# Kernel optimization log

Measured on AMD Instinct MI355X. Metric: run time of the kernel, lower is better.

## Reference

```python
import jax, jax.numpy as jnp
import numpy as np
import math

B, T, EMB, HD = 4, 2048, 2048, 128
HALF = HD // 2


def setup_inputs() -> dict:
    key = jax.random.key(0)
    ks = jax.random.split(key, 4)
    x = jax.random.normal(ks[0], (B, T, EMB), dtype=jnp.float32)
    s = 1.0 / math.sqrt(EMB)
    Wq = jax.random.normal(ks[1], (EMB, HD), dtype=jnp.float32) * s
    Wk = jax.random.normal(ks[2], (EMB, HD), dtype=jnp.float32) * s
    Wv = jax.random.normal(ks[3], (EMB, HD), dtype=jnp.float32) * s
    # Standard RoPE rotation table: theta_i = 10000^(-2i/HD), angle = pos * theta
    inv_freq = 1.0 / (10000.0 ** (np.arange(0, HALF, dtype=np.float32) / HALF))
    angles = np.arange(T, dtype=np.float32)[:, None] * inv_freq[None, :]  # [T, HALF]
    rot_cos = jnp.asarray(np.cos(angles), dtype=jnp.float32)
    rot_sin = jnp.asarray(np.sin(angles), dtype=jnp.float32)
    # Additive causal mask: 0 on/below diagonal, -1e9 above
    NEG = -1e9
    mask = jnp.where(jnp.tril(jnp.ones((T, T), dtype=bool)), 0.0, NEG).astype(jnp.float32)
    return {"x": x, "Wq": Wq, "Wk": Wk, "Wv": Wv,
            "rot_cos": rot_cos, "rot_sin": rot_sin, "mask": mask}


def _apply_rope(q, rot_cos, rot_sin):
    # q: [B, T, HD]; view last dim as HALF complex pairs and rotate
    qp = q.reshape(q.shape[0], q.shape[1], HALF, 2)
    re, im = qp[..., 0], qp[..., 1]
    out_re = re * rot_cos - im * rot_sin  # broadcast [T,HALF] over batch
    out_im = re * rot_sin + im * rot_cos
    return jnp.stack([out_re, out_im], axis=-1).reshape(q.shape)


def reference(x, Wq, Wk, Wv, rot_cos, rot_sin, mask):
    Q = x @ Wq  # [B, T, HD]
    K = x @ Wk
    V = x @ Wv
    Q = _apply_rope(Q, rot_cos, rot_sin)
    K = _apply_rope(K, rot_cos, rot_sin)
    scores = jnp.einsum('bqd,bkd->bqk', Q, K) / math.sqrt(HD)
    probs = jax.nn.softmax(scores + mask, axis=-1)  # dropout is identity in eval
    return jnp.einsum('bqk,bkd->bqd', probs, V)
```

## Files before the change

kernel.cpp:

```cpp
#include <hip/hip_runtime.h>
#include <cstddef>
#include <cstdint>

#define T_SEQ 2048
#define EMB_D 2048
#define HD_D  128

typedef __attribute__((ext_vector_type(8))) short short8;
typedef __attribute__((ext_vector_type(4))) float f32x4;
typedef __attribute__((ext_vector_type(4))) unsigned short ushort4v;
typedef __attribute__((ext_vector_type(8))) unsigned short ushort8v;
typedef __attribute__((ext_vector_type(2))) unsigned int uint2v;

static __device__ __forceinline__ unsigned short f2bf_rne(float f) {
    union { float f; unsigned u; } v; v.f = f;
    unsigned r = v.u + 0x7fffu + ((v.u >> 16) & 1u);
    return (unsigned short)(r >> 16);
}
static __device__ __forceinline__ unsigned short f2bf_fast(float f) {
    union { float f; unsigned u; } v; v.f = f;
    return (unsigned short)((v.u + 0x8000u) >> 16);
}
static __device__ __forceinline__ float bf2f(unsigned short h) {
    union { unsigned u; float f; } v; v.u = ((unsigned)h) << 16;
    return v.f;
}
static __device__ __forceinline__ unsigned pk2(float a, float b) {
    union { float f; unsigned u; } x, y; x.f = a; y.f = b;
    return __builtin_amdgcn_perm(y.u + 0x8000u, x.u + 0x8000u, 0x07060302);
}
#define EXP2F(x) __builtin_amdgcn_exp2f(x)

__global__ __launch_bounds__(256) void prep_weights(
    const float* __restrict__ Wq, const float* __restrict__ Wk,
    const float* __restrict__ Wv, unsigned short* __restrict__ Wt)
{
    __shared__ __attribute__((aligned(16))) unsigned short tw[64 * 132];
    const int w = blockIdx.y;
    const int k0 = blockIdx.x * 64;
    const float* W = (w == 0) ? Wq : (w == 1) ? Wk : Wv;
    const int tid = threadIdx.x;
#pragma unroll
    for (int p = 0; p < 8; p++) {
        const int f = p * 256 + tid;
        const int row = f >> 5, c4 = f & 31;
        const float4 v = *(const float4*)&W[(size_t)(k0 + row) * HD_D + c4 * 4];
        ushort4v h = { f2bf_rne(v.x), f2bf_rne(v.y), f2bf_rne(v.z), f2bf_rne(v.w) };
        *(ushort4v*)&tw[row * 132 + c4 * 4] = h;
    }
    __syncthreads();
    const int kk = (tid & 7) * 8;
#pragma unroll
    for (int p = 0; p < 4; p++) {
        const int n = p * 32 + (tid >> 3);
        ushort8v o;
#pragma unroll
        for (int jj = 0; jj < 8; jj++) o[jj] = tw[(kk + jj) * 132 + n];
        *(ushort8v*)&Wt[(size_t)w * (HD_D * EMB_D) + (size_t)n * EMB_D + k0 + kk] = o;
    }
}

__global__ __launch_bounds__(256, 2) void qkv_fused(
    const float* __restrict__ x, const unsigned short* __restrict__ Wt,
    const float* __restrict__ rcos, const float* __restrict__ rsin,
    unsigned short* __restrict__ Qb, unsigned short* __restrict__ Kb,
    unsigned short* __restrict__ Vt)
{
    __shared__ __attribute__((aligned(16))) unsigned short xsm[2][64 * 64];
    __shared__ __attribute__((aligned(16))) unsigned short wsm[2][96 * 64];
    const int L = blockIdx.x;
    const int xcd = L & 7, s = L >> 3;
    const int ng = s & 3;
    const int m0 = (xcd * 16 + (s >> 2)) * 64;
    const int tid = threadIdx.x;
    const int lane = tid & 63, wave = tid >> 6;
    const int wm = wave >> 1, wn = wave & 1;
    const int l15 = lane & 15, lq = lane >> 4;

    const int xrow = tid >> 4, xc = tid & 15;
    const float* xsrc = x + (size_t)(m0 + xrow) * EMB_D + xc * 4;
    const int wrow = tid >> 3, wc = tid & 7;
    const unsigned short* wsrc = Wt + (size_t)(ng * 96 + wrow) * EMB_D + wc * 8;

    const int xw  = xrow * 128 + (((xc >> 1) ^ (xrow & 7)) << 4) + (xc & 1) * 8;
    const int wwo = wrow * 128 + ((wc ^ (wrow & 7)) << 4);

    int ra[2][2], rb[3][2];
#pragma unroll
    for (int i = 0; i < 2; i++)
#pragma unroll
        for (int ks = 0; ks < 2; ks++) {
            const int row = wm * 32 + i * 16 + l15;
            ra[i][ks] = row * 128 + (((ks * 4 + lq) ^ (row & 7)) << 4);
        }
#pragma unroll
    for (int jj = 0; jj < 3; jj++)
#pragma unroll
        for (int ks = 0; ks < 2; ks++) {
            const int row = wn * 48 + jj * 16 + l15;
            rb[jj][ks] = row * 128 + (((ks * 4 + lq) ^ (row & 7)) << 4);
        }

    f32x4 acc[2][3];
#pragma unroll
    for (int i = 0; i < 2; i++)
#pragma unroll
        for (int j = 0; j < 3; j++) acc[i][j] = (f32x4){0.f, 0.f, 0.f, 0.f};

    float4 xr[2][4];
    short8 wr[2][3];

#define LOADN(SET, K)                                                             \
    do {                                                                          \
        _Pragma("unroll")                                                         \
        for (int p = 0; p < 4; p++)                                               \
            xr[SET][p] = *(const float4*)(xsrc + (size_t)p * (16 * EMB_D) + (K)); \
        _Pragma("unroll")                                                         \
        for (int p = 0; p < 3; p++)                                               \
            wr[SET][p] = *(const short8*)(wsrc + (size_t)p * (32 * EMB_D) + (K)); \
    } while (0)

#define STAGE(SET, BUF)                                                           \
    do {                                                                          \
        char* xb = (char*)&xsm[BUF][0];                                           \
        char* wb = (char*)&wsm[BUF][0];                                           \
        _Pragma("unroll")                                                         \
        for (int p = 0; p < 4; p++) {                                             \
            uint2v u;                                                             \
            u.x = pk2(xr[SET][p].x, xr[SET][p].y);                                \
            u.y = pk2(xr[SET][p].z, xr[SET][p].w);                                \
            *(uint2v*)(xb + xw + p * 2048) = u;                                   \
        }                                                                         \
        _Pragma("unroll")                                                         \
        for (int p = 0; p < 3; p++)                                               \
            *(short8*)(wb + wwo + p * 4096) = wr[SET][p];                         \
    } while (0)

#define COMPUTE(BUF)                                                              \
    do {                                                                          \
        const char* xb = (const char*)&xsm[BUF][0];                               \
        const char* wb = (const char*)&wsm[BUF][0];                               \
        short8 Af[2][2];                                                          \
        _Pragma("unroll")                                                         \
        for (int i = 0; i < 2; i++)                                               \
            _Pragma("unroll")                                                     \
            for (int ks = 0; ks < 2; ks++)                                        \
                Af[i][ks] = *(const short8*)(xb + ra[i][ks]);                     \
        __builtin_amdgcn_s_setprio(1);                                            \
        _Pragma("unroll")                                                         \
        for (int ks = 0; ks < 2; ks++)                                            \
            _Pragma("unroll")                                                     \
            for (int jj = 0; jj < 3; jj++) {                                      \
                const short8 Bf = *(const short8*)(wb + rb[jj][ks]);              \
                _Pragma("unroll")                                                 \
                for (int i = 0; i < 2; i++)                                       \
                    acc[i][jj] = __builtin_amdgcn_mfma_f32_16x16x32_bf16(         \
                        Af[i][ks], Bf, acc[i][jj], 0, 0, 0);                      \
            }                                                                     \
        __builtin_amdgcn_s_setprio(0);                                            \
    } while (0)

#define BARX() asm volatile("s_waitcnt lgkmcnt(0)\n\ts_barrier" ::: "memory")

    LOADN(0, 0);
    LOADN(1, 64);
    STAGE(0, 0);
    LOADN(0, 128);

#pragma clang loop unroll(disable)
    for (int j = 0; j < 28; j += 2) {
        BARX(); STAGE(1, 1); LOADN(1, (j + 3) * 64); COMPUTE(0);
        BARX(); STAGE(0, 0); LOADN(0, (j + 4) * 64); COMPUTE(1);
    }
    BARX(); STAGE(1, 1); LOADN(1, 31 * 64); COMPUTE(0);
    BARX(); STAGE(0, 0);                    COMPUTE(1);
    BARX(); STAGE(1, 1);                    COMPUTE(0);
    BARX();                                 COMPUTE(1);

#undef LOADN
#undef STAGE
#undef COMPUTE
#undef BARX

    const float qscale = 0.08838834764831845f * 1.4426950408889634f;
#pragma unroll
    for (int i = 0; i < 2; i++) {
#pragma unroll
        for (int r = 0; r < 4; r++) {
            const int row = m0 + wm * 32 + i * 16 + lq * 4 + r;
            const int t = row & (T_SEQ - 1);
            const int bb = row >> 11;
#pragma unroll
            for (int j = 0; j < 3; j++) {
                const int col = ng * 96 + wn * 48 + j * 16 + l15;
                const int mat = col >> 7, mcol = col & 127;
                const float v = acc[i][j][r];
                if (mat == 2) {
                    Vt[((size_t)bb * HD_D + mcol) * T_SEQ + t] = f2bf_rne(v);
                } else {
                    const int ip = mcol >> 1;
                    const float c = rcos[t * 64 + ip];
                    const float s2 = rsin[t * 64 + ip];
                    const float pv = __shfl_xor(v, 1);
                    float rv = (mcol & 1) ? (pv * s2 + v * c) : (v * c - pv * s2);
                    if (mat == 0) {
                        rv *= qscale;
                        Qb[(size_t)row * HD_D + mcol] = f2bf_rne(rv);
                    } else {
                        Kb[(size_t)row * HD_D + mcol] = f2bf_rne(rv);
                    }
                }
            }
        }
    }
}

__global__ __launch_bounds__(256, 2) void attn(
    const unsigned short* __restrict__ Qb, const unsigned short* __restrict__ Kb,
    const unsigned short* __restrict__ Vt, float* __restrict__ O0,
    unsigned short* __restrict__ O1, float* __restrict__ Lp)
{
    __shared__ __attribute__((aligned(16))) unsigned short O_s[4][16 * 128];
    __shared__ __attribute__((aligned(16))) unsigned short P_s[4][2][16 * 40];
    __shared__ float l_s[4][16];

    const int tid = threadIdx.x;
    const int lane = tid & 63, wave = tid >> 6;
    const int l15 = lane & 15, lq = lane >> 4;
    const int kf = lq * 8;

    const int L = blockIdx.x;
    const int g = L & 1;
    const int b = (L >> 1) & 3;
    const int q0 = (127 - (L >> 3)) * 16;
    const int kend = q0 + 16;
    const float M2 = 16.0f;

    const unsigned short* Qp = Qb + (size_t)(b * T_SEQ + q0) * HD_D;
    short8 aQ[4];
#pragma unroll
    for (int d = 0; d < 4; d++)
        aQ[d] = *(const short8*)&Qp[l15 * HD_D + d * 32 + kf];

    f32x4 acc[8];
#pragma unroll
    for (int d = 0; d < 8; d++) acc[d] = (f32x4){0.f, 0.f, 0.f, 0.f};
    float l_r[4] = {0.f, 0.f, 0.f, 0.f};

    const unsigned short* Kbase = Kb + (size_t)b * T_SEQ * HD_D;
    const unsigned short* Vbase = Vt + (size_t)b * HD_D * T_SEQ;
    unsigned short* PwA = &P_s[wave][0][0];
    unsigned short* PwB = &P_s[wave][1][0];

    for (int c = 2 * wave + g; c * 32 < kend; c += 16) {
        const int kA = c * 32;
        const int kB = (c + 8) * 32;
        const bool hB = kB < kend;

        const unsigned short* KpA = Kbase + (size_t)kA * HD_D;
        const unsigned short* KpB = Kbase + (size_t)kB * HD_D;
        short8 KA[8], KB_[8];
#pragma unroll
        for (int d = 0; d < 4; d++)
#pragma unroll
            for (int n = 0; n < 2; n++)
                KA[d * 2 + n] = *(const short8*)&KpA[(size_t)(n * 16 + l15) * HD_D + d * 32 + kf];
        if (hB) {
#pragma unroll
            for (int d = 0; d < 4; d++)
#pragma unroll
                for (int n = 0; n < 2; n++)
                    KB_[d * 2 + n] = *(const short8*)&KpB[(size_t)(n * 16 + l15) * HD_D + d * 32 + kf];
        }

        f32x4 sA0 = (f32x4){0.f, 0.f, 0.f, 0.f}, sA1 = sA0, sB0 = sA0, sB1 = sA0;
#pragma unroll
        for (int d = 0; d < 4; d++) {
            sA0 = __builtin_amdgcn_mfma_f32_16x16x32_bf16(aQ[d], KA[d * 2 + 0], sA0, 0, 0, 0);
            sA1 = __builtin_amdgcn_mfma_f32_16x16x32_bf16(aQ[d], KA[d * 2 + 1], sA1, 0, 0, 0);
        }
        if (hB) {
#pragma unroll
            for (int d = 0; d < 4; d++) {
                sB0 = __builtin_amdgcn_mfma_f32_16x16x32_bf16(aQ[d], KB_[d * 2 + 0], sB0, 0, 0, 0);
                sB1 = __builtin_amdgcn_mfma_f32_16x16x32_bf16(aQ[d], KB_[d * 2 + 1], sB1, 0, 0, 0);
            }
        }

        short8 VA[8];
#pragma unroll
        for (int d = 0; d < 8; d++)
            VA[d] = *(const short8*)&Vbase[(size_t)(d * 16 + l15) * T_SEQ + kA + kf];

#pragma unroll
        for (int r = 0; r < 4; r++) {
            const int q = q0 + lq * 4 + r;
            const float p0 = ((kA + l15)      <= q) ? EXP2F(sA0[r] - M2) : 0.f;
            const float p1 = ((kA + 16 + l15) <= q) ? EXP2F(sA1[r] - M2) : 0.f;
            l_r[r] += p0 + p1;
            const int prow = (lq * 4 + r) * 40;
            PwA[prow + l15]      = f2bf_fast(p0);
            PwA[prow + 16 + l15] = f2bf_fast(p1);
        }
        const short8 pA = *(const short8*)&PwA[l15 * 40 + kf];
#pragma unroll
        for (int d = 0; d < 8; d++)
            acc[d] = __builtin_amdgcn_mfma_f32_16x16x32_bf16(pA, VA[d], acc[d], 0, 0, 0);

        if (hB) {
            short8 VB[8];
#pragma unroll
            for (int d = 0; d < 8; d++)
                VB[d] = *(const short8*)&Vbase[(size_t)(d * 16 + l15) * T_SEQ + kB + kf];
#pragma unroll
            for (int r = 0; r < 4; r++) {
                const int q = q0 + lq * 4 + r;
                const float p0 = ((kB + l15)      <= q) ? EXP2F(sB0[r] - M2) : 0.f;
                const float p1 = ((kB + 16 + l15) <= q) ? EXP2F(sB1[r] - M2) : 0.f;
                l_r[r] += p0 + p1;
                const int prow = (lq * 4 + r) * 40;
                PwB[prow + l15]      = f2bf_fast(p0);
                PwB[prow + 16 + l15] = f2bf_fast(p1);
            }
            const short8 pB = *(const short8*)&PwB[l15 * 40 + kf];
#pragma unroll
            for (int d = 0; d < 8; d++)
                acc[d] = __builtin_amdgcn_mfma_f32_16x16x32_bf16(pB, VB[d], acc[d], 0, 0, 0);
        }
    }

#pragma unroll
    for (int r = 0; r < 4; r++) {
        float lr = l_r[r];
        lr += __shfl_xor(lr, 1);
        lr += __shfl_xor(lr, 2);
        lr += __shfl_xor(lr, 4);
        lr += __shfl_xor(lr, 8);
        if (l15 == 0) l_s[wave][lq * 4 + r] = lr;
#pragma unroll
        for (int d = 0; d < 8; d++)
            O_s[wave][(lq * 4 + r) * 128 + d * 16 + l15] = f2bf_fast(acc[d][r]);
    }
    __syncthreads();

    const int row = tid >> 4;
    const int dc = (tid & 15) * 8;
    const float lt = l_s[0][row] + l_s[1][row] + l_s[2][row] + l_s[3][row];
    float o[8];
#pragma unroll
    for (int k = 0; k < 8; k++) o[k] = 0.f;
#pragma unroll
    for (int w2 = 0; w2 < 4; w2++) {
        const ushort8v pv = *(const ushort8v*)&O_s[w2][row * 128 + dc];
#pragma unroll
        for (int k = 0; k < 8; k++) o[k] += bf2f(pv[k]);
    }
    const size_t grow = (size_t)(b * T_SEQ + q0 + row);
    if (g == 0) {
        float* op = O0 + grow * HD_D + dc;
#pragma unroll
        for (int k = 0; k < 8; k++) op[k] = o[k];
    } else {
        ushort8v h;
#pragma unroll
        for (int k = 0; k < 8; k++) h[k] = f2bf_fast(o[k]);
        *(ushort8v*)&O1[grow * HD_D + dc] = h;
    }
    if ((tid & 15) == 0) Lp[g * 8192 + grow] = lt;
}

__global__ __launch_bounds__(256) void attn_merge(
    float* __restrict__ out, const unsigned short* __restrict__ O1,
    const float* __restrict__ Lp)
{
    const int idx = blockIdx.x * 256 + threadIdx.x;
    const int row = idx >> 5;
    f32x4 a = ((f32x4*)out)[idx];
    const ushort4v h = ((const ushort4v*)O1)[idx];
    f32x4 bv = { bf2f(h.x), bf2f(h.y), bf2f(h.z), bf2f(h.w) };
    const float inv = 1.0f / (Lp[row] + Lp[8192 + row]);
    ((f32x4*)out)[idx] = (a + bv) * inv;
}

extern "C" void kernel_launch(void* const* d_in, const int* in_sizes, int n_in,
                              void* d_out, int out_size, void* d_ws, size_t ws_size,
                              hipStream_t stream)
{
    (void)in_sizes; (void)n_in; (void)out_size; (void)ws_size;
    const float* x  = (const float*)d_in[0];
    const float* Wq = (const float*)d_in[1];
    const float* Wk = (const float*)d_in[2];
    const float* Wv = (const float*)d_in[3];
    const float* rc = (const float*)d_in[4];
    const float* rs = (const float*)d_in[5];
    float* out = (float*)d_out;

    char* ws = (char*)d_ws;
    unsigned short* Wt = (unsigned short*)(ws);
    unsigned short* Qb = (unsigned short*)(ws + 1572864);
    unsigned short* Kb = (unsigned short*)(ws + 3670016);
    unsigned short* Vt = (unsigned short*)(ws + 5767168);
    unsigned short* O1 = (unsigned short*)(ws + 7864320);
    float*          Lp = (float*)(ws + 9961472);

    prep_weights<<<dim3(32, 3), 256, 0, stream>>>(Wq, Wk, Wv, Wt);
    qkv_fused   <<<dim3(512),   256, 0, stream>>>(x, Wt, rc, rs, Qb, Kb, Vt);
    attn        <<<dim3(1024),  256, 0, stream>>>(Qb, Kb, Vt, out, O1, Lp);
    attn_merge  <<<dim3(1024),  256, 0, stream>>>(out, O1, Lp);
}
```

Baseline: 179.9 us.

## Enlarge attention query tile to 32 rows and software-pipeline K loads

Each attention block now handles 32 query rows instead of 16, so every K and V fragment loaded from global memory feeds two MFMA row tiles. The grid is halved to 512 blocks to match. The key loop is restructured with ping-pong K register buffers so the next chunk's K load is issued before the current chunk's softmax and PV step. The cost is more registers (double accumulators and two K buffers) at launch bounds of 2 blocks per CU, fewer blocks for load balancing across the causal triangle, and coarser masking work on the diagonal.

```diff
diff --git a/kernel.cpp b/kernel.cpp
--- a/kernel.cpp
+++ b/kernel.cpp
@@ -220,9 +220,9 @@
     const unsigned short* __restrict__ Vt, float* __restrict__ O0,
     unsigned short* __restrict__ O1, float* __restrict__ Lp)
 {
-    __shared__ __attribute__((aligned(16))) unsigned short O_s[4][16 * 128];
-    __shared__ __attribute__((aligned(16))) unsigned short P_s[4][2][16 * 40];
-    __shared__ float l_s[4][16];
+    __shared__ __attribute__((aligned(16))) unsigned short O_s[4][32 * 128];
+    __shared__ __attribute__((aligned(16))) unsigned short P_s[4][32 * 40];
+    __shared__ float l_s[4][32];
 
     const int tid = threadIdx.x;
     const int lane = tid & 63, wave = tid >> 6;
@@ -232,141 +232,169 @@
     const int L = blockIdx.x;
     const int g = L & 1;
     const int b = (L >> 1) & 3;
-    const int q0 = (127 - (L >> 3)) * 16;
-    const int kend = q0 + 16;
+    const int q0 = (63 - (L >> 3)) * 32;
+    const int kend = q0 + 32;
     const float M2 = 16.0f;
 
     const unsigned short* Qp = Qb + (size_t)(b * T_SEQ + q0) * HD_D;
-    short8 aQ[4];
-#pragma unroll
-    for (int d = 0; d < 4; d++)
-        aQ[d] = *(const short8*)&Qp[l15 * HD_D + d * 32 + kf];
-
-    f32x4 acc[8];
-#pragma unroll
-    for (int d = 0; d < 8; d++) acc[d] = (f32x4){0.f, 0.f, 0.f, 0.f};
-    float l_r[4] = {0.f, 0.f, 0.f, 0.f};
+    short8 aQ[2][4];
+#pragma unroll
+    for (int i = 0; i < 2; i++)
+#pragma unroll
+        for (int d = 0; d < 4; d++)
+            aQ[i][d] = *(const short8*)&Qp[(size_t)(i * 16 + l15) * HD_D + d * 32 + kf];
+
+    f32x4 acc[2][8];
+#pragma unroll
+    for (int i = 0; i < 2; i++)
+#pragma unroll
+        for (int d = 0; d < 8; d++) acc[i][d] = (f32x4){0.f, 0.f, 0.f, 0.f};
+    float l_r[2][4] = {{0.f, 0.f, 0.f, 0.f}, {0.f, 0.f, 0.f, 0.f}};
 
     const unsigned short* Kbase = Kb + (size_t)b * T_SEQ * HD_D;
     const unsigned short* Vbase = Vt + (size_t)b * HD_D * T_SEQ;
-    unsigned short* PwA = &P_s[wave][0][0];
-    unsigned short* PwB = &P_s[wave][1][0];
-
-    for (int c = 2 * wave + g; c * 32 < kend; c += 16) {
-        const int kA = c * 32;
-        const int kB = (c + 8) * 32;
-        const bool hB = kB < kend;
-
-        const unsigned short* KpA = Kbase + (size_t)kA * HD_D;
-        const unsigned short* KpB = Kbase + (size_t)kB * HD_D;
-        short8 KA[8], KB_[8];
-#pragma unroll
-        for (int d = 0; d < 4; d++)
-#pragma unroll
-            for (int n = 0; n < 2; n++)
-                KA[d * 2 + n] = *(const short8*)&KpA[(size_t)(n * 16 + l15) * HD_D + d * 32 + kf];
-        if (hB) {
-#pragma unroll
-            for (int d = 0; d < 4; d++)
-#pragma unroll
-                for (int n = 0; n < 2; n++)
-                    KB_[d * 2 + n] = *(const short8*)&KpB[(size_t)(n * 16 + l15) * HD_D + d * 32 + kf];
-        }
-
-        f32x4 sA0 = (f32x4){0.f, 0.f, 0.f, 0.f}, sA1 = sA0, sB0 = sA0, sB1 = sA0;
-#pragma unroll
-        for (int d = 0; d < 4; d++) {
-            sA0 = __builtin_amdgcn_mfma_f32_16x16x32_bf16(aQ[d], KA[d * 2 + 0], sA0, 0, 0, 0);
-            sA1 = __builtin_amdgcn_mfma_f32_16x16x32_bf16(aQ[d], KA[d * 2 + 1], sA1, 0, 0, 0);
-        }
-        if (hB) {
-#pragma unroll
-            for (int d = 0; d < 4; d++) {
-                sB0 = __builtin_amdgcn_mfma_f32_16x16x32_bf16(aQ[d], KB_[d * 2 + 0], sB0, 0, 0, 0);
-                sB1 = __builtin_amdgcn_mfma_f32_16x16x32_bf16(aQ[d], KB_[d * 2 + 1], sB1, 0, 0, 0);
+    unsigned short* Pw = &P_s[wave][0];
+
+    short8 KA_A[8], KA_B[8], VA[8];
+    f32x4 sc[2][2];
+
+#define LOADK(DST, C0)                                                         \
+    do {                                                                       \
+        const unsigned short* Kp = Kbase + (size_t)((C0) * 32) * HD_D;         \
+        _Pragma("unroll")                                                      \
+        for (int d = 0; d < 4; d++)                                            \
+            _Pragma("unroll")                                                  \
+            for (int n = 0; n < 2; n++)                                        \
+                DST[d * 2 + n] =                                               \
+                    *(const short8*)&Kp[(size_t)(n * 16 + l15) * HD_D + d * 32 + kf]; \
+    } while (0)
+
+#define QKSEG(KREG)                                                            \
+    do {                                                                       \
+        _Pragma("unroll")                                                      \
+        for (int i = 0; i < 2; i++)                                            \
+            _Pragma("unroll")                                                  \
+            for (int n = 0; n < 2; n++) sc[i][n] = (f32x4){0.f, 0.f, 0.f, 0.f};\
+        _Pragma("unroll")                                                      \
+        for (int d = 0; d < 4; d++)                                            \
+            _Pragma("unroll")                                                  \
+            for (int i = 0; i < 2; i++)                                        \
+                _Pragma("unroll")                                              \
+                for (int n = 0; n < 2; n++)                                    \
+                    sc[i][n] = __builtin_amdgcn_mfma_f32_16x16x32_bf16(        \
+                        aQ[i][d], KREG[d * 2 + n], sc[i][n], 0, 0, 0);         \
+    } while (0)
+
+#define LOADV(C0)                                                              \
+    do {                                                                       \
+        _Pragma("unroll")                                                      \
+        for (int d = 0; d < 8; d++)                                            \
+            VA[d] = *(const short8*)                                           \
+                &Vbase[(size_t)(d * 16 + l15) * T_SEQ + (C0) * 32 + kf];       \
+    } while (0)
+
+#define SMPV(C0)                                                               \
+    do {                                                                       \
+        const int kA = (C0) * 32;                                              \
+        _Pragma("unroll")                                                      \
+        for (int i = 0; i < 2; i++)                                            \
+            _Pragma("unroll")                                                  \
+            for (int r = 0; r < 4; r++) {                                      \
+                const int q = q0 + i * 16 + lq * 4 + r;                        \
+                const float p0 = ((kA + l15)      <= q) ? EXP2F(sc[i][0][r] - M2) : 0.f; \
+                const float p1 = ((kA + 16 + l15) <= q) ? EXP2F(sc[i][1][r] - M2) : 0.f; \
+                l_r[i][r] += p0 + p1;                                          \
+                const int prow = (i * 16 + lq * 4 + r) * 40;                   \
+                Pw[prow + l15]      = f2bf_fast(p0);                           \
+                Pw[prow + 16 + l15] = f2bf_fast(p1);                           \
+            }                                                                  \
+        short8 pA[2];                                                          \
+        _Pragma("unroll")                                                      \
+        for (int i = 0; i < 2; i++)                                            \
+            pA[i] = *(const short8*)&Pw[(i * 16 + l15) * 40 + kf];             \
+        _Pragma("unroll")                                                      \
+        for (int i = 0; i < 2; i++)                                            \
+            _Pragma("unroll")                                                  \
+            for (int d = 0; d < 8; d++)                                        \
+                acc[i][d] = __builtin_amdgcn_mfma_f32_16x16x32_bf16(           \
+                    pA[i], VA[d], acc[i][d], 0, 0, 0);                         \
+    } while (0)
+
+    int cc = 2 * wave + g;
+    if (cc * 32 < kend) {
+        LOADK(KA_A, cc);
+#pragma clang loop unroll(disable)
+        for (;;) {
+            QKSEG(KA_A);
+            LOADV(cc);
+            {
+                const int cB = cc + 8;
+                const bool hB = (cB * 32 < kend);
+                if (hB) LOADK(KA_B, cB);
+                SMPV(cc);
+                if (!hB) break;
             }
-        }
-
-        short8 VA[8];
-#pragma unroll
-        for (int d = 0; d < 8; d++)
-            VA[d] = *(const short8*)&Vbase[(size_t)(d * 16 + l15) * T_SEQ + kA + kf];
-
+            QKSEG(KA_B);
+            LOADV(cc + 8);
+            {
+                const int cC = cc + 16;
+                const bool hC = (cC * 32 < kend);
+                if (hC) LOADK(KA_A, cC);
+                SMPV(cc + 8);
+                if (!hC) break;
+            }
+            cc += 16;
+        }
+    }
+
+#undef LOADK
+#undef QKSEG
+#undef LOADV
+#undef SMPV
+
+#pragma unroll
+    for (int i = 0; i < 2; i++)
 #pragma unroll
         for (int r = 0; r < 4; r++) {
-            const int q = q0 + lq * 4 + r;
-            const float p0 = ((kA + l15)      <= q) ? EXP2F(sA0[r] - M2) : 0.f;
-            const float p1 = ((kA + 16 + l15) <= q) ? EXP2F(sA1[r] - M2) : 0.f;
-            l_r[r] += p0 + p1;
-            const int prow = (lq * 4 + r) * 40;
-            PwA[prow + l15]      = f2bf_fast(p0);
-            PwA[prow + 16 + l15] = f2bf_fast(p1);
-        }
-        const short8 pA = *(const short8*)&PwA[l15 * 40 + kf];
-#pragma unroll
-        for (int d = 0; d < 8; d++)
-            acc[d] = __builtin_amdgcn_mfma_f32_16x16x32_bf16(pA, VA[d], acc[d], 0, 0, 0);
-
-        if (hB) {
-            short8 VB[8];
+            float lr = l_r[i][r];
+            lr += __shfl_xor(lr, 1);
+            lr += __shfl_xor(lr, 2);
+            lr += __shfl_xor(lr, 4);
+            lr += __shfl_xor(lr, 8);
+            if (l15 == 0) l_s[wave][i * 16 + lq * 4 + r] = lr;
 #pragma unroll
             for (int d = 0; d < 8; d++)
-                VB[d] = *(const short8*)&Vbase[(size_t)(d * 16 + l15) * T_SEQ + kB + kf];
-#pragma unroll
-            for (int r = 0; r < 4; r++) {
-                const int q = q0 + lq * 4 + r;
-                const float p0 = ((kB + l15)      <= q) ? EXP2F(sB0[r] - M2) : 0.f;
-                const float p1 = ((kB + 16 + l15) <= q) ? EXP2F(sB1[r] - M2) : 0.f;
-                l_r[r] += p0 + p1;
-                const int prow = (lq * 4 + r) * 40;
-                PwB[prow + l15]      = f2bf_fast(p0);
-                PwB[prow + 16 + l15] = f2bf_fast(p1);
-            }
-            const short8 pB = *(const short8*)&PwB[l15 * 40 + kf];
-#pragma unroll
-            for (int d = 0; d < 8; d++)
-                acc[d] = __builtin_amdgcn_mfma_f32_16x16x32_bf16(pB, VB[d], acc[d], 0, 0, 0);
-        }
-    }
-
-#pragma unroll
-    for (int r = 0; r < 4; r++) {
-        float lr = l_r[r];
-        lr += __shfl_xor(lr, 1);
-        lr += __shfl_xor(lr, 2);
-        lr += __shfl_xor(lr, 4);
-        lr += __shfl_xor(lr, 8);
-        if (l15 == 0) l_s[wave][lq * 4 + r] = lr;
-#pragma unroll
-        for (int d = 0; d < 8; d++)
-            O_s[wave][(lq * 4 + r) * 128 + d * 16 + l15] = f2bf_fast(acc[d][r]);
-    }
+                O_s[wave][(i * 16 + lq * 4 + r) * 128 + d * 16 + l15] = f2bf_fast(acc[i][d][r]);
+        }
     __syncthreads();
 
-    const int row = tid >> 4;
-    const int dc = (tid & 15) * 8;
-    const float lt = l_s[0][row] + l_s[1][row] + l_s[2][row] + l_s[3][row];
-    float o[8];
-#pragma unroll
-    for (int k = 0; k < 8; k++) o[k] = 0.f;
-#pragma unroll
-    for (int w2 = 0; w2 < 4; w2++) {
-        const ushort8v pv = *(const ushort8v*)&O_s[w2][row * 128 + dc];
-#pragma unroll
-        for (int k = 0; k < 8; k++) o[k] += bf2f(pv[k]);
-    }
-    const size_t grow = (size_t)(b * T_SEQ + q0 + row);
-    if (g == 0) {
-        float* op = O0 + grow * HD_D + dc;
-#pragma unroll
-        for (int k = 0; k < 8; k++) op[k] = o[k];
-    } else {
-        ushort8v h;
-#pragma unroll
-        for (int k = 0; k < 8; k++) h[k] = f2bf_fast(o[k]);
-        *(ushort8v*)&O1[grow * HD_D + dc] = h;
-    }
-    if ((tid & 15) == 0) Lp[g * 8192 + grow] = lt;
+#pragma unroll
+    for (int pass = 0; pass < 2; pass++) {
+        const int row = pass * 16 + (tid >> 4);
+        const int dc = (tid & 15) * 8;
+        const float lt = l_s[0][row] + l_s[1][row] + l_s[2][row] + l_s[3][row];
+        float o[8];
+#pragma unroll
+        for (int k = 0; k < 8; k++) o[k] = 0.f;
+#pragma unroll
+        for (int w2 = 0; w2 < 4; w2++) {
+            const ushort8v pv = *(const ushort8v*)&O_s[w2][row * 128 + dc];
+#pragma unroll
+            for (int k = 0; k < 8; k++) o[k] += bf2f(pv[k]);
+        }
+        const size_t grow = (size_t)(b * T_SEQ + q0 + row);
+        if (g == 0) {
+            float* op = O0 + grow * HD_D + dc;
+#pragma unroll
+            for (int k = 0; k < 8; k++) op[k] = o[k];
+        } else {
+            ushort8v h;
+#pragma unroll
+            for (int k = 0; k < 8; k++) h[k] = f2bf_fast(o[k]);
+            *(ushort8v*)&O1[grow * HD_D + dc] = h;
+        }
+        if ((tid & 15) == 0) Lp[g * 8192 + grow] = lt;
+    }
 }
 
 __global__ __launch_bounds__(256) void attn_merge(
@@ -405,6 +433,6 @@
 
     prep_weights<<<dim3(32, 3), 256, 0, stream>>>(Wq, Wk, Wv, Wt);
     qkv_fused   <<<dim3(512),   256, 0, stream>>>(x, Wt, rc, rs, Qb, Kb, Vt);
-    attn        <<<dim3(1024),  256, 0, stream>>>(Qb, Kb, Vt, out, O1, Lp);
+    attn        <<<dim3(512),   256, 0, stream>>>(Qb, Kb, Vt, out, O1, Lp);
     attn_merge  <<<dim3(1024),  256, 0, stream>>>(out, O1, Lp);
 }
```

After: 172.4 us, median of 2. -4.2%, faster.
